# Kernel optimization log

Measured on AMD Instinct MI355X. Metric: run time of the kernel, lower is better.

Reference implementation:

```python
import jax, jax.numpy as jnp
import numpy as np

N_MLP = 1024  # number of independent tiny MLPs
D_IN, D_HID, D_OUT = 2, 4, 1
B = 16384


def setup_inputs() -> dict:
    key = jax.random.key(0)
    k = jax.random.split(key, 6)
    x = jax.random.normal(k[0], (B, N_MLP), dtype=jnp.float32)
    x_aug = jax.random.normal(k[1], (B, N_MLP), dtype=jnp.float32)
    # Stacked per-MLP parameters (nn.Linear default init ~ U(-1/sqrt(fan_in), 1/sqrt(fan_in)))
    s1 = 1.0 / np.sqrt(D_IN)
    s2 = 1.0 / np.sqrt(D_HID)
    W1 = jax.random.uniform(k[2], (N_MLP, D_HID, D_IN), jnp.float32, -s1, s1)
    b1 = jax.random.uniform(k[3], (N_MLP, D_HID), jnp.float32, -s1, s1)
    W2 = jax.random.uniform(k[4], (N_MLP, D_OUT, D_HID), jnp.float32, -s2, s2)
    b2 = jax.random.uniform(k[5], (N_MLP, D_OUT), jnp.float32, -s2, s2)
    return {"x": x, "x_aug": x_aug, "W1": W1, "b1": b1, "W2": W2, "b2": b2}


def reference(x, x_aug, W1, b1, W2, b2):
    # data: [B, N, 2] — pair (original, augmented) per feature
    data = jnp.stack([x, x_aug], axis=-1)
    # batched tiny GEMM across the N_MLP axis: [B,N,2] x [N,4,2] -> [B,N,4]
    h = jax.nn.relu(jnp.einsum('bne,nhe->bnh', data, W1) + b1)
    # [B,N,4] x [N,1,4] -> [B,N,1]
    o = jnp.einsum('bnh,noh->bno', h, W2) + b2
    # concat over dim1 of per-MLP [B,1] outputs == squeeze -> [B,N]; mean over N -> [B]
    return jnp.mean(o[..., 0], axis=1)
```

## Files before the change

kernel.cpp:

```cpp
#include <hip/hip_runtime.h>


constexpr int N_MLP = 1024;
constexpr int BATCH = 16384;
constexpr int ROWS = 8;
constexpr int NTHREADS = 256;
constexpr int QN = 256;
constexpr int NQ = N_MLP / QN;

typedef __attribute__((address_space(3))) void lds_void;
typedef const __attribute__((address_space(1))) void gbl_void;

__global__ __launch_bounds__(256)
void zero_out_kernel(float* __restrict__ out) {
    out[blockIdx.x * 256 + threadIdx.x] = 0.0f;
}

__global__ __launch_bounds__(NTHREADS, 8)
void disc_mlp_kernel(const float* __restrict__ x,
                     const float* __restrict__ xa,
                     const float* __restrict__ W1,
                     const float* __restrict__ b1,
                     const float* __restrict__ W2,
                     const float* __restrict__ b2,
                     float* __restrict__ out)
{
    __shared__ float xbuf[ROWS * QN];
    __shared__ float abuf[ROWS * QN];
    __shared__ float red[NTHREADS / 64][ROWS];

    const int t    = threadIdx.x;
    const int lane = t & 63;
    const int wave = t >> 6;
    const int q  = blockIdx.x & (NQ - 1);
    const int rb = blockIdx.x >> 2;
    const int b0 = rb * ROWS;
    const int n  = q * QN + t;

    const float4 p0 = reinterpret_cast<const float4*>(W1)[(size_t)n * 2];
    const float4 p1 = reinterpret_cast<const float4*>(W1)[(size_t)n * 2 + 1];
    const float4 bb = reinterpret_cast<const float4*>(b1)[n];
    const float4 ww = reinterpret_cast<const float4*>(W2)[n];
    const float  b2r = b2[n];

    const float* gx = x  + (size_t)b0 * N_MLP + q * QN;
    const float* ga = xa + (size_t)b0 * N_MLP + q * QN;
#pragma unroll
    for (int i = 0; i < ROWS / 4; ++i) {
        const int r = wave * (ROWS / 4) + i;
        const float* srcx = gx + (size_t)r * N_MLP + lane * 4;
        const float* srca = ga + (size_t)r * N_MLP + lane * 4;
        __builtin_amdgcn_global_load_lds((gbl_void*)srcx,
                                         (lds_void*)&xbuf[r * QN + lane * 4],
                                         16, 0, 0);
        __builtin_amdgcn_global_load_lds((gbl_void*)srca,
                                         (lds_void*)&abuf[r * QN + lane * 4],
                                         16, 0, 0);
    }
    __syncthreads();

    const float A[4]   = {p0.x, p0.z, p1.x, p1.z};
    const float C[4]   = {p0.y, p0.w, p1.y, p1.w};
    const float B1r[4] = {bb.x, bb.y, bb.z, bb.w};
    const float V[4]   = {ww.x, ww.y, ww.z, ww.w};

    float acc[ROWS];
#pragma unroll
    for (int r = 0; r < ROWS; ++r) {
        const float xe  = xbuf[r * QN + t];
        const float xae = abuf[r * QN + t];
        float s = b2r;
#pragma unroll
        for (int j = 0; j < 4; ++j) {
            float h = fmaf(A[j], xe, fmaf(C[j], xae, B1r[j]));
            h = fmaxf(h, 0.0f);
            s = fmaf(V[j], h, s);
        }
        acc[r] = s;
    }

#pragma unroll
    for (int r = 0; r < ROWS; ++r) {
        float v = acc[r];
        v += __shfl_down(v, 32);
        v += __shfl_down(v, 16);
        v += __shfl_down(v, 8);
        v += __shfl_down(v, 4);
        v += __shfl_down(v, 2);
        v += __shfl_down(v, 1);
        if (lane == 0) red[wave][r] = v;
    }
    __syncthreads();
    if (t < ROWS) {
        float s = (red[0][t] + red[1][t]) + (red[2][t] + red[3][t]);
        atomicAdd(out + b0 + t, s * (1.0f / (float)N_MLP));
    }
}

extern "C" void kernel_launch(void* const* d_in, const int* in_sizes, int n_in,
                              void* d_out, int out_size, void* d_ws, size_t ws_size,
                              hipStream_t stream) {
    const float* x  = (const float*)d_in[0];
    const float* xa = (const float*)d_in[1];
    const float* W1 = (const float*)d_in[2];
    const float* b1 = (const float*)d_in[3];
    const float* W2 = (const float*)d_in[4];
    const float* b2 = (const float*)d_in[5];
    float* out = (float*)d_out;

    zero_out_kernel<<<BATCH / 256, 256, 0, stream>>>(out);
    disc_mlp_kernel<<<(BATCH / ROWS) * NQ, NTHREADS, 0, stream>>>(x, xa, W1, b1, W2, b2, out);
}
```

Measured before the change: 148.5 us.

## Use persistent blocks with double-buffered LDS prefetch of input tiles

```diff
diff --git a/kernel.cpp b/kernel.cpp
--- a/kernel.cpp
+++ b/kernel.cpp
@@ -3,10 +3,13 @@
 
 constexpr int N_MLP = 1024;
 constexpr int BATCH = 16384;
-constexpr int ROWS = 8;
+constexpr int ROWS = 4;
 constexpr int NTHREADS = 256;
 constexpr int QN = 256;
 constexpr int NQ = N_MLP / QN;
+constexpr int NBLK = 2048;
+constexpr int GROUPS = NBLK / NQ;
+constexpr int TILES = (BATCH / ROWS) / GROUPS;
 
 typedef __attribute__((address_space(3))) void lds_void;
 typedef const __attribute__((address_space(1))) void gbl_void;
@@ -25,17 +28,15 @@
                      const float* __restrict__ b2,
                      float* __restrict__ out)
 {
-    __shared__ float xbuf[ROWS * QN];
-    __shared__ float abuf[ROWS * QN];
-    __shared__ float red[NTHREADS / 64][ROWS];
+    __shared__ float xbuf[2][ROWS * QN];
+    __shared__ float abuf[2][ROWS * QN];
 
     const int t    = threadIdx.x;
     const int lane = t & 63;
     const int wave = t >> 6;
-    const int q  = blockIdx.x & (NQ - 1);
-    const int rb = blockIdx.x >> 2;
-    const int b0 = rb * ROWS;
-    const int n  = q * QN + t;
+    const int q    = blockIdx.x & (NQ - 1);
+    const int g    = blockIdx.x >> 2;
+    const int n    = q * QN + t;
 
     const float4 p0 = reinterpret_cast<const float4*>(W1)[(size_t)n * 2];
     const float4 p1 = reinterpret_cast<const float4*>(W1)[(size_t)n * 2 + 1];
@@ -43,57 +44,63 @@
     const float4 ww = reinterpret_cast<const float4*>(W2)[n];
     const float  b2r = b2[n];
 
-    const float* gx = x  + (size_t)b0 * N_MLP + q * QN;
-    const float* ga = xa + (size_t)b0 * N_MLP + q * QN;
-#pragma unroll
-    for (int i = 0; i < ROWS / 4; ++i) {
-        const int r = wave * (ROWS / 4) + i;
-        const float* srcx = gx + (size_t)r * N_MLP + lane * 4;
-        const float* srca = ga + (size_t)r * N_MLP + lane * 4;
-        __builtin_amdgcn_global_load_lds((gbl_void*)srcx,
-                                         (lds_void*)&xbuf[r * QN + lane * 4],
-                                         16, 0, 0);
-        __builtin_amdgcn_global_load_lds((gbl_void*)srca,
-                                         (lds_void*)&abuf[r * QN + lane * 4],
-                                         16, 0, 0);
-    }
-    __syncthreads();
-
     const float A[4]   = {p0.x, p0.z, p1.x, p1.z};
     const float C[4]   = {p0.y, p0.w, p1.y, p1.w};
     const float B1r[4] = {bb.x, bb.y, bb.z, bb.w};
     const float V[4]   = {ww.x, ww.y, ww.z, ww.w};
 
-    float acc[ROWS];
+    const float* gx = x  + q * QN;
+    const float* ga = xa + q * QN;
+
+    auto stage = [&](int it, int buf) {
+        const int b0 = (g + it * GROUPS) * ROWS;
+        const size_t off = (size_t)(b0 + wave) * N_MLP + lane * 4;
+        __builtin_amdgcn_global_load_lds((gbl_void*)(gx + off),
+                                         (lds_void*)&xbuf[buf][wave * QN + lane * 4],
+                                         16, 0, 0);
+        __builtin_amdgcn_global_load_lds((gbl_void*)(ga + off),
+                                         (lds_void*)&abuf[buf][wave * QN + lane * 4],
+                                         16, 0, 0);
+    };
+
+    stage(0, 0);
+    __syncthreads();
+
+    for (int it = 0; it < TILES; ++it) {
+        const int cur = it & 1;
+        if (it + 1 < TILES) stage(it + 1, cur ^ 1);
+
+        const int b0 = (g + it * GROUPS) * ROWS;
+
+        float acc[ROWS];
 #pragma unroll
-    for (int r = 0; r < ROWS; ++r) {
-        const float xe  = xbuf[r * QN + t];
-        const float xae = abuf[r * QN + t];
-        float s = b2r;
+        for (int r = 0; r < ROWS; ++r) {
+            const float xe  = xbuf[cur][r * QN + t];
+            const float xae = abuf[cur][r * QN + t];
+            float s = b2r;
 #pragma unroll
-        for (int j = 0; j < 4; ++j) {
-            float h = fmaf(A[j], xe, fmaf(C[j], xae, B1r[j]));
-            h = fmaxf(h, 0.0f);
-            s = fmaf(V[j], h, s);
+            for (int j = 0; j < 4; ++j) {
+                float h = fmaf(A[j], xe, fmaf(C[j], xae, B1r[j]));
+                h = fmaxf(h, 0.0f);
+                s = fmaf(V[j], h, s);
+            }
+            acc[r] = s;
         }
-        acc[r] = s;
-    }
 
 #pragma unroll
-    for (int r = 0; r < ROWS; ++r) {
-        float v = acc[r];
-        v += __shfl_down(v, 32);
-        v += __shfl_down(v, 16);
-        v += __shfl_down(v, 8);
-        v += __shfl_down(v, 4);
-        v += __shfl_down(v, 2);
-        v += __shfl_down(v, 1);
-        if (lane == 0) red[wave][r] = v;
-    }
-    __syncthreads();
-    if (t < ROWS) {
-        float s = (red[0][t] + red[1][t]) + (red[2][t] + red[3][t]);
-        atomicAdd(out + b0 + t, s * (1.0f / (float)N_MLP));
+        for (int r = 0; r < ROWS; ++r) {
+            float v = acc[r];
+            v += __shfl_down(v, 32);
+            v += __shfl_down(v, 16);
+            v += __shfl_down(v, 8);
+            v += __shfl_down(v, 4);
+            v += __shfl_down(v, 2);
+            v += __shfl_down(v, 1);
+            if (lane == 0)
+                atomicAdd(out + b0 + r, v * (1.0f / (float)N_MLP));
+        }
+
+        __syncthreads();
     }
 }
 
@@ -109,5 +116,5 @@
     float* out = (float*)d_out;
 
     zero_out_kernel<<<BATCH / 256, 256, 0, stream>>>(out);
-    disc_mlp_kernel<<<(BATCH / ROWS) * NQ, NTHREADS, 0, stream>>>(x, xa, W1, b1, W2, b2, out);
+    disc_mlp_kernel<<<NBLK, NTHREADS, 0, stream>>>(x, xa, W1, b1, W2, b2, out);
 }
```

After: 161.9 us. 9.1% more time.

## Process two MLPs per thread and loop over two row tiles per block

Applied to the files above, without the earlier changes.

```diff
diff --git a/kernel.cpp b/kernel.cpp
--- a/kernel.cpp
+++ b/kernel.cpp
@@ -5,8 +5,11 @@
 constexpr int BATCH = 16384;
 constexpr int ROWS = 8;
 constexpr int NTHREADS = 256;
-constexpr int QN = 256;
+constexpr int K = 2;
+constexpr int QN = NTHREADS * K;
 constexpr int NQ = N_MLP / QN;
+constexpr int TILES = 2;
+constexpr int NBLK = (BATCH / (ROWS * TILES)) * NQ;
 
 typedef __attribute__((address_space(3))) void lds_void;
 typedef const __attribute__((address_space(1))) void gbl_void;
@@ -16,7 +19,7 @@
     out[blockIdx.x * 256 + threadIdx.x] = 0.0f;
 }
 
-__global__ __launch_bounds__(NTHREADS, 8)
+__global__ __launch_bounds__(NTHREADS, 4)
 void disc_mlp_kernel(const float* __restrict__ x,
                      const float* __restrict__ xa,
                      const float* __restrict__ W1,
@@ -32,68 +35,86 @@
     const int t    = threadIdx.x;
     const int lane = t & 63;
     const int wave = t >> 6;
-    const int q  = blockIdx.x & (NQ - 1);
-    const int rb = blockIdx.x >> 2;
-    const int b0 = rb * ROWS;
-    const int n  = q * QN + t;
+    const int q    = blockIdx.x & (NQ - 1);
+    const int g    = blockIdx.x >> 1;
+    const int n0   = q * QN + t * K;
 
-    const float4 p0 = reinterpret_cast<const float4*>(W1)[(size_t)n * 2];
-    const float4 p1 = reinterpret_cast<const float4*>(W1)[(size_t)n * 2 + 1];
-    const float4 bb = reinterpret_cast<const float4*>(b1)[n];
-    const float4 ww = reinterpret_cast<const float4*>(W2)[n];
-    const float  b2r = b2[n];
+    const float4 wa0 = reinterpret_cast<const float4*>(W1)[(size_t)n0 * 2];
+    const float4 wb0 = reinterpret_cast<const float4*>(W1)[(size_t)n0 * 2 + 1];
+    const float4 wa1 = reinterpret_cast<const float4*>(W1)[(size_t)(n0 + 1) * 2];
+    const float4 wb1 = reinterpret_cast<const float4*>(W1)[(size_t)(n0 + 1) * 2 + 1];
+    const float4 b10 = reinterpret_cast<const float4*>(b1)[n0];
+    const float4 b11 = reinterpret_cast<const float4*>(b1)[n0 + 1];
+    const float4 w20 = reinterpret_cast<const float4*>(W2)[n0];
+    const float4 w21 = reinterpret_cast<const float4*>(W2)[n0 + 1];
+    const float2 b2v = reinterpret_cast<const float2*>(b2)[n0 >> 1];
+    const float bsum = b2v.x + b2v.y;
 
-    const float* gx = x  + (size_t)b0 * N_MLP + q * QN;
-    const float* ga = xa + (size_t)b0 * N_MLP + q * QN;
-#pragma unroll
-    for (int i = 0; i < ROWS / 4; ++i) {
-        const int r = wave * (ROWS / 4) + i;
-        const float* srcx = gx + (size_t)r * N_MLP + lane * 4;
-        const float* srca = ga + (size_t)r * N_MLP + lane * 4;
-        __builtin_amdgcn_global_load_lds((gbl_void*)srcx,
-                                         (lds_void*)&xbuf[r * QN + lane * 4],
-                                         16, 0, 0);
-        __builtin_amdgcn_global_load_lds((gbl_void*)srca,
-                                         (lds_void*)&abuf[r * QN + lane * 4],
-                                         16, 0, 0);
-    }
-    __syncthreads();
+    const float* gx = x  + q * QN;
+    const float* ga = xa + q * QN;
 
-    const float A[4]   = {p0.x, p0.z, p1.x, p1.z};
-    const float C[4]   = {p0.y, p0.w, p1.y, p1.w};
-    const float B1r[4] = {bb.x, bb.y, bb.z, bb.w};
-    const float V[4]   = {ww.x, ww.y, ww.z, ww.w};
-
-    float acc[ROWS];
-#pragma unroll
-    for (int r = 0; r < ROWS; ++r) {
-        const float xe  = xbuf[r * QN + t];
-        const float xae = abuf[r * QN + t];
-        float s = b2r;
-#pragma unroll
-        for (int j = 0; j < 4; ++j) {
-            float h = fmaf(A[j], xe, fmaf(C[j], xae, B1r[j]));
-            h = fmaxf(h, 0.0f);
-            s = fmaf(V[j], h, s);
-        }
-        acc[r] = s;
-    }
+    for (int it = 0; it < TILES; ++it) {
+        const int b0 = (g * TILES + it) * ROWS;
 
 #pragma unroll
-    for (int r = 0; r < ROWS; ++r) {
-        float v = acc[r];
-        v += __shfl_down(v, 32);
-        v += __shfl_down(v, 16);
-        v += __shfl_down(v, 8);
-        v += __shfl_down(v, 4);
-        v += __shfl_down(v, 2);
-        v += __shfl_down(v, 1);
-        if (lane == 0) red[wave][r] = v;
-    }
-    __syncthreads();
-    if (t < ROWS) {
-        float s = (red[0][t] + red[1][t]) + (red[2][t] + red[3][t]);
-        atomicAdd(out + b0 + t, s * (1.0f / (float)N_MLP));
+        for (int i = 0; i < ROWS / 4; ++i) {
+            const int r = wave * (ROWS / 4) + i;
+#pragma unroll
+            for (int c = 0; c < QN / 256; ++c) {
+                const size_t off = (size_t)(b0 + r) * N_MLP + c * 256 + lane * 4;
+                __builtin_amdgcn_global_load_lds(
+                    (gbl_void*)(gx + off),
+                    (lds_void*)&xbuf[r * QN + c * 256 + lane * 4], 16, 0, 0);
+                __builtin_amdgcn_global_load_lds(
+                    (gbl_void*)(ga + off),
+                    (lds_void*)&abuf[r * QN + c * 256 + lane * 4], 16, 0, 0);
+            }
+        }
+        __syncthreads();
+
+        const float2* xb = reinterpret_cast<const float2*>(xbuf);
+        const float2* ab = reinterpret_cast<const float2*>(abuf);
+        float acc[ROWS];
+#pragma unroll
+        for (int r = 0; r < ROWS; ++r) {
+            const float2 xv = xb[r * (QN / 2) + t];
+            const float2 av = ab[r * (QN / 2) + t];
+            float s = bsum;
+            float h0 = fmaf(wa0.x, xv.x, fmaf(wa0.y, av.x, b10.x));
+            float h1 = fmaf(wa0.z, xv.x, fmaf(wa0.w, av.x, b10.y));
+            float h2 = fmaf(wb0.x, xv.x, fmaf(wb0.y, av.x, b10.z));
+            float h3 = fmaf(wb0.z, xv.x, fmaf(wb0.w, av.x, b10.w));
+            s = fmaf(w20.x, fmaxf(h0, 0.0f), s);
+            s = fmaf(w20.y, fmaxf(h1, 0.0f), s);
+            s = fmaf(w20.z, fmaxf(h2, 0.0f), s);
+            s = fmaf(w20.w, fmaxf(h3, 0.0f), s);
+            h0 = fmaf(wa1.x, xv.y, fmaf(wa1.y, av.y, b11.x));
+            h1 = fmaf(wa1.z, xv.y, fmaf(wa1.w, av.y, b11.y));
+            h2 = fmaf(wb1.x, xv.y, fmaf(wb1.y, av.y, b11.z));
+            h3 = fmaf(wb1.z, xv.y, fmaf(wb1.w, av.y, b11.w));
+            s = fmaf(w21.x, fmaxf(h0, 0.0f), s);
+            s = fmaf(w21.y, fmaxf(h1, 0.0f), s);
+            s = fmaf(w21.z, fmaxf(h2, 0.0f), s);
+            s = fmaf(w21.w, fmaxf(h3, 0.0f), s);
+            acc[r] = s;
+        }
+
+#pragma unroll
+        for (int r = 0; r < ROWS; ++r) {
+            float v = acc[r];
+            v += __shfl_down(v, 32);
+            v += __shfl_down(v, 16);
+            v += __shfl_down(v, 8);
+            v += __shfl_down(v, 4);
+            v += __shfl_down(v, 2);
+            v += __shfl_down(v, 1);
+            if (lane == 0) red[wave][r] = v;
+        }
+        __syncthreads();
+        if (t < ROWS) {
+            float s = (red[0][t] + red[1][t]) + (red[2][t] + red[3][t]);
+            atomicAdd(out + b0 + t, s * (1.0f / (float)N_MLP));
+        }
     }
 }
 
@@ -109,5 +130,5 @@
     float* out = (float*)d_out;
 
     zero_out_kernel<<<BATCH / 256, 256, 0, stream>>>(out);
-    disc_mlp_kernel<<<(BATCH / ROWS) * NQ, NTHREADS, 0, stream>>>(x, xa, W1, b1, W2, b2, out);
+    disc_mlp_kernel<<<NBLK, NTHREADS, 0, stream>>>(x, xa, W1, b1, W2, b2, out);
 }
```

Measured after the change: 154.8 us. 1.04x slower.
